# Performance work log

Hardware: AMD Instinct MI355X
Metric: run time of the kernel (lower is better)

## Reference

```python
import jax, jax.numpy as jnp
import numpy as np

N_NODES = 100000


def high_pass_filter(z, src, dst, n):
    # add self loops (PyG add_self_loops appends [i, i] edges)
    loop = jnp.arange(n, dtype=src.dtype)
    src2 = jnp.concatenate([src, loop])
    dst2 = jnp.concatenate([dst, loop])
    ones = jnp.ones(src2.shape[0], dtype=z.dtype)
    # deg = degree(edge_index[0]) -> out-degree counts per source node
    deg = jax.ops.segment_sum(ones, src2, num_segments=n)
    # mean aggregation at target nodes: out[i] = mean_{(j->i)} z[j]
    msg_sum = jax.ops.segment_sum(z[src2], dst2, num_segments=n)
    cnt = jax.ops.segment_sum(ones, dst2, num_segments=n)
    mean_out = msg_sum / cnt[:, None]  # cnt >= 1 thanks to self loops
    return z - mean_out / deg[:, None]


def setup_inputs() -> dict:
    key = jax.random.key(0)
    k = jax.random.split(key, 8)
    d = 64
    E = 1200000
    x = jax.random.normal(k[0], (N_NODES, d), dtype=jnp.float32)
    edge_index = jax.random.randint(k[1], (2, E), 0, N_NODES, dtype=jnp.int64)
    s = 1.0 / np.sqrt(d)
    W1 = jax.random.uniform(k[2], (d, d), jnp.float32, -s, s)
    b1 = jax.random.uniform(k[3], (d,), jnp.float32, -s, s)
    W2 = jax.random.uniform(k[4], (d, d), jnp.float32, -s, s)
    b2 = jax.random.uniform(k[5], (d,), jnp.float32, -s, s)
    W3 = jax.random.uniform(k[6], (d, d), jnp.float32, -s, s)
    b3 = jax.random.uniform(k[7], (d,), jnp.float32, -s, s)
    return {"x": x, "edge_index": edge_index, "W1": W1, "b1": b1,
            "W2": W2, "b2": b2, "W3": W3, "b3": b3}


def reference(x, edge_index, W1, b1, W2, b2, W3, b3):
    src, dst = edge_index[0], edge_index[1]
    n = x.shape[0]
    z = jax.nn.relu(x @ W1 + b1)
    z = high_pass_filter(z, src, dst, n)
    z = jax.nn.relu(z @ W2 + b2)
    z = high_pass_filter(z, src, dst, n)
    z = jax.nn.relu(z @ W3 + b3)
    return z
```

## Files before the change

kernel.cpp:

```cpp
#include <hip/hip_runtime.h>

#define D 64
#define CAP 48
#define CAPB 3584
#define BIN_CHUNK 2048

typedef unsigned int uint;
typedef unsigned short ushort;

__device__ __forceinline__ ushort f2bf(float f) {
    uint u = __float_as_uint(f);
    return (ushort)((u + 0x7FFFu + ((u >> 16) & 1u)) >> 16);
}

__global__ __launch_bounds__(256) void k_bin2(
    const int* __restrict__ src, const int* __restrict__ dst, int E, int nb,
    int* __restrict__ gcur, int* __restrict__ binD, int* __restrict__ binS)
{
    __shared__ int curD[512], curS[512];
    const int t = threadIdx.x;
    for (int i = t; i < nb; i += 256) { curD[i] = 0; curS[i] = 0; }
    __syncthreads();

    const int e0 = blockIdx.x * BIN_CHUNK;
    int sv[8], dv[8];
#pragma unroll
    for (int i = 0; i < 8; ++i) {
        int e = e0 + i * 256 + t;
        if (e < E) {
            sv[i] = src[e]; dv[i] = dst[e];
            atomicAdd(&curD[dv[i] >> 8], 1);
            atomicAdd(&curS[sv[i] >> 8], 1);
        } else {
            sv[i] = -1;
        }
    }
    __syncthreads();
    for (int i = t; i < nb; i += 256) {
        int c = curD[i]; curD[i] = c ? atomicAdd(&gcur[i], c) : 0;
        c = curS[i];     curS[i] = c ? atomicAdd(&gcur[nb + i], c) : 0;
    }
    __syncthreads();
#pragma unroll
    for (int i = 0; i < 8; ++i) {
        if (sv[i] >= 0) {
            int b = dv[i] >> 8;
            int pos = atomicAdd(&curD[b], 1);
            if (pos < CAPB) binD[(size_t)b * CAPB + pos] = ((dv[i] & 255) << 17) | sv[i];
            b = sv[i] >> 8;
            pos = atomicAdd(&curS[b], 1);
            if (pos < CAPB) binS[(size_t)b * CAPB + pos] = sv[i] & 255;
        }
    }
}

__global__ __launch_bounds__(256) void k_finish(
    const int* __restrict__ gcur, const int* __restrict__ binD,
    const int* __restrict__ binS, int n, int nb,
    int* __restrict__ csr, int* __restrict__ icnt, float* __restrict__ inv)
{
    __shared__ int cur[256], od[256];
    const int b = blockIdx.x, t = threadIdx.x;
    cur[t] = 0; od[t] = 0;
    __syncthreads();

    int cntD = gcur[b]; if (cntD > CAPB) cntD = CAPB;
    const int* bb = binD + (size_t)b * CAPB;
    for (int i = t; i < cntD; i += 256) {
        int v = bb[i];
        int dloc = v >> 17;
        int pos = atomicAdd(&cur[dloc], 1);
        if (pos < CAP) csr[(size_t)((b << 8) + dloc) * CAP + pos] = v & 0x1FFFF;
    }
    int cntS = gcur[nb + b]; if (cntS > CAPB) cntS = CAPB;
    const int* bs = binS + (size_t)b * CAPB;
    for (int i = t; i < cntS; i += 256) {
        atomicAdd(&od[bs[i]], 1);
    }
    __syncthreads();
    int node = (b << 8) + t;
    if (node < n) {
        int ic = cur[t]; if (ic > CAP) ic = CAP;
        icnt[node] = ic;
        inv[node] = 1.0f / ((float)(od[t] + 1) * (float)(ic + 1));
    }
}

__global__ __launch_bounds__(256) void k_aggr(
    const float* __restrict__ zA, const ushort* __restrict__ zh,
    const int* __restrict__ icnt, const int* __restrict__ csr,
    const float* __restrict__ inv, int n, float* __restrict__ zB)
{
    int w = (blockIdx.x * 256 + threadIdx.x) >> 6;
    int lane = threadIdx.x & 63;
    int c8 = (lane & 7) << 3;
    int j = lane >> 3;
    if (w >= n) return;

    int cnt = icnt[w]; if (cnt > CAP) cnt = CAP;
    int my = (lane < cnt) ? csr[w * CAP + lane] : 0;
    int nit = (cnt + 7) >> 3;

    float a[8] = {0.f, 0.f, 0.f, 0.f, 0.f, 0.f, 0.f, 0.f};
    for (int it = 0; it < nit; ++it) {
        int e = (it << 3) + j;
        int s = __shfl(my, e, 64);
        uint4 u = *(const uint4*)(zh + (size_t)s * D + c8);
        if (e < cnt) {
            a[0] += __uint_as_float(u.x << 16);
            a[1] += __uint_as_float(u.x & 0xFFFF0000u);
            a[2] += __uint_as_float(u.y << 16);
            a[3] += __uint_as_float(u.y & 0xFFFF0000u);
            a[4] += __uint_as_float(u.z << 16);
            a[5] += __uint_as_float(u.z & 0xFFFF0000u);
            a[6] += __uint_as_float(u.w << 16);
            a[7] += __uint_as_float(u.w & 0xFFFF0000u);
        }
    }
#pragma unroll
    for (int m = 8; m <= 32; m <<= 1) {
#pragma unroll
        for (int i = 0; i < 8; ++i) a[i] += __shfl_xor(a[i], m, 64);
    }

    if (j == 0) {
        float iv = inv[w];
        const float* zr = zA + (size_t)w * D + c8;
        float4 s0 = *(const float4*)zr;
        float4 s1 = *(const float4*)(zr + 4);
        float4 o0, o1;
        o0.x = fmaf(-(a[0] + s0.x), iv, s0.x);
        o0.y = fmaf(-(a[1] + s0.y), iv, s0.y);
        o0.z = fmaf(-(a[2] + s0.z), iv, s0.z);
        o0.w = fmaf(-(a[3] + s0.w), iv, s0.w);
        o1.x = fmaf(-(a[4] + s1.x), iv, s1.x);
        o1.y = fmaf(-(a[5] + s1.y), iv, s1.y);
        o1.z = fmaf(-(a[6] + s1.z), iv, s1.z);
        o1.w = fmaf(-(a[7] + s1.w), iv, s1.w);
        float* zo = zB + (size_t)w * D + c8;
        *(float4*)zo = o0;
        *(float4*)(zo + 4) = o1;
    }
}

#define LDS_STRIDE 68

__global__ __launch_bounds__(256) void k_gemm(
    const float* z, const float* __restrict__ W, const float* __restrict__ bias,
    float* out, ushort* zh_out, int n)
{
    __shared__ float sX[64 * LDS_STRIDE];
    __shared__ float sWT[64 * LDS_STRIDE];

    const int t = threadIdx.x;
    const int row0 = blockIdx.x * 64;

    for (int i = 0; i < 4; ++i) {
        int s = i * 256 + t;
        int k = s >> 4;
        int c4 = (s & 15) << 2;
        float4 w = ((const float4*)W)[s];
        sWT[(c4 + 0) * LDS_STRIDE + k] = w.x;
        sWT[(c4 + 1) * LDS_STRIDE + k] = w.y;
        sWT[(c4 + 2) * LDS_STRIDE + k] = w.z;
        sWT[(c4 + 3) * LDS_STRIDE + k] = w.w;
    }
    for (int i = 0; i < 4; ++i) {
        int s = i * 256 + t;
        int r = s >> 4;
        int grow = row0 + r;
        float4 v = make_float4(0.f, 0.f, 0.f, 0.f);
        if (grow < n) v = ((const float4*)(z + (size_t)grow * D))[s & 15];
        *((float4*)(sX + r * LDS_STRIDE + ((s & 15) << 2))) = v;
    }
    __syncthreads();

    const int tc = (t & 15) << 2;
    const int tr = (t >> 4) << 2;

    float acc[4][4] = {};
#define DOT4(a_, w_, acc_) \
    acc_ = fmaf((a_).x, (w_).x, fmaf((a_).y, (w_).y, fmaf((a_).z, (w_).z, fmaf((a_).w, (w_).w, acc_))))

    for (int k4 = 0; k4 < 16; ++k4) {
        float4 a0 = *(const float4*)(sX + (tr + 0) * LDS_STRIDE + (k4 << 2));
        float4 a1 = *(const float4*)(sX + (tr + 1) * LDS_STRIDE + (k4 << 2));
        float4 a2 = *(const float4*)(sX + (tr + 2) * LDS_STRIDE + (k4 << 2));
        float4 a3 = *(const float4*)(sX + (tr + 3) * LDS_STRIDE + (k4 << 2));
        float4 w0 = *(const float4*)(sWT + (tc + 0) * LDS_STRIDE + (k4 << 2));
        float4 w1 = *(const float4*)(sWT + (tc + 1) * LDS_STRIDE + (k4 << 2));
        float4 w2 = *(const float4*)(sWT + (tc + 2) * LDS_STRIDE + (k4 << 2));
        float4 w3 = *(const float4*)(sWT + (tc + 3) * LDS_STRIDE + (k4 << 2));
        DOT4(a0, w0, acc[0][0]); DOT4(a0, w1, acc[0][1]); DOT4(a0, w2, acc[0][2]); DOT4(a0, w3, acc[0][3]);
        DOT4(a1, w0, acc[1][0]); DOT4(a1, w1, acc[1][1]); DOT4(a1, w2, acc[1][2]); DOT4(a1, w3, acc[1][3]);
        DOT4(a2, w0, acc[2][0]); DOT4(a2, w1, acc[2][1]); DOT4(a2, w2, acc[2][2]); DOT4(a2, w3, acc[2][3]);
        DOT4(a3, w0, acc[3][0]); DOT4(a3, w1, acc[3][1]); DOT4(a3, w2, acc[3][2]); DOT4(a3, w3, acc[3][3]);
    }

    float b0 = bias[tc + 0], b1 = bias[tc + 1], b2 = bias[tc + 2], b3 = bias[tc + 3];
    for (int rr = 0; rr < 4; ++rr) {
        int grow = row0 + tr + rr;
        if (grow >= n) continue;
        float4 o;
        o.x = fmaxf(acc[rr][0] + b0, 0.f);
        o.y = fmaxf(acc[rr][1] + b1, 0.f);
        o.z = fmaxf(acc[rr][2] + b2, 0.f);
        o.w = fmaxf(acc[rr][3] + b3, 0.f);
        ((float4*)(out + (size_t)grow * D))[tc >> 2] = o;
        if (zh_out) {
            short4 h;
            h.x = (short)f2bf(o.x); h.y = (short)f2bf(o.y);
            h.z = (short)f2bf(o.z); h.w = (short)f2bf(o.w);
            *(short4*)(zh_out + (size_t)grow * D + tc) = h;
        }
    }
}

extern "C" void kernel_launch(void* const* d_in, const int* in_sizes, int n_in,
                              void* d_out, int out_size, void* d_ws, size_t ws_size,
                              hipStream_t stream) {
    const float* x  = (const float*)d_in[0];
    const int*   ei = (const int*)d_in[1];
    const float* W1 = (const float*)d_in[2];
    const float* b1 = (const float*)d_in[3];
    const float* W2 = (const float*)d_in[4];
    const float* b2 = (const float*)d_in[5];
    const float* W3 = (const float*)d_in[6];
    const float* b3 = (const float*)d_in[7];

    const int n = in_sizes[0] / D;
    const int E = in_sizes[1] / 2;
    const int* src = ei;
    const int* dst = ei + E;

    const int nb = (n + 255) >> 8;

    float*  zA   = (float*)d_ws;
    ushort* zh   = (ushort*)(zA + (size_t)n * D);
    float*  inv  = (float*)(zh + (size_t)n * D);
    int*    icnt = (int*)(inv + n);
    int*    csr  = icnt + n;
    int*    gcur = csr + (size_t)n * CAP;
    int*    binD = gcur + 2 * nb;
    int*    binS = binD + (size_t)nb * CAPB;

    float* out = (float*)d_out;
    dim3 blk(256);

    hipMemsetAsync(gcur, 0, 2 * (size_t)nb * sizeof(int), stream);

    const int bin_blocks = (E + BIN_CHUNK - 1) / BIN_CHUNK;
    k_bin2<<<dim3(bin_blocks), blk, 0, stream>>>(src, dst, E, nb, gcur, binD, binS);
    k_finish<<<dim3(nb), blk, 0, stream>>>(gcur, binD, binS, n, nb, csr, icnt, inv);

    dim3 gemm_grid((n + 63) / 64);
    dim3 aggr_grid((n + 3) / 4);

    k_gemm<<<gemm_grid, blk, 0, stream>>>(x, W1, b1, zA, zh, n);
    k_aggr<<<aggr_grid, blk, 0, stream>>>(zA, zh, icnt, csr, inv, n, zA);
    k_gemm<<<gemm_grid, blk, 0, stream>>>(zA, W2, b2, zA, zh, n);
    k_aggr<<<aggr_grid, blk, 0, stream>>>(zA, zh, icnt, csr, inv, n, zA);
    k_gemm<<<gemm_grid, blk, 0, stream>>>(zA, W3, b3, out, nullptr, n);
}
```

Before: 294.3 us.

## Merge edge binning and first GEMM into one launch, replace memset with kernel

Edge binning and the first dense layer are independent, so they now run as two halves of one grid, with block index choosing the role. This lets them overlap and removes one launch. The hipMemsetAsync is replaced by a tiny zeroing kernel, and the aggregation kernel issues its self-row and inverse-degree loads before the neighbor loop to hide latency. The cost is a larger shared-memory allocation for the binning blocks, which may lower their occupancy.

```diff
diff --git a/kernel.cpp b/kernel.cpp
--- a/kernel.cpp
+++ b/kernel.cpp
@@ -4,6 +4,7 @@
 #define CAP 48
 #define CAPB 3584
 #define BIN_CHUNK 2048
+#define LDS_STRIDE 68
 
 typedef unsigned int uint;
 typedef unsigned short ushort;
@@ -13,16 +14,21 @@
     return (ushort)((u + 0x7FFFu + ((u >> 16) & 1u)) >> 16);
 }
 
-__global__ __launch_bounds__(256) void k_bin2(
-    const int* __restrict__ src, const int* __restrict__ dst, int E, int nb,
-    int* __restrict__ gcur, int* __restrict__ binD, int* __restrict__ binS)
-{
-    __shared__ int curD[512], curS[512];
+__global__ void k_zero(int* __restrict__ p, int n) {
+    int i = blockIdx.x * blockDim.x + threadIdx.x;
+    if (i < n) p[i] = 0;
+}
+
+__device__ void bin2_body(const int* __restrict__ src, const int* __restrict__ dst,
+                          int E, int nb, int* __restrict__ gcur,
+                          int* __restrict__ binD, int* __restrict__ binS,
+                          int* curD, int* curS, int chunk)
+{
     const int t = threadIdx.x;
     for (int i = t; i < nb; i += 256) { curD[i] = 0; curS[i] = 0; }
     __syncthreads();
 
-    const int e0 = blockIdx.x * BIN_CHUNK;
+    const int e0 = chunk * BIN_CHUNK;
     int sv[8], dv[8];
 #pragma unroll
     for (int i = 0; i < 8; ++i) {
@@ -54,106 +60,12 @@
     }
 }
 
-__global__ __launch_bounds__(256) void k_finish(
-    const int* __restrict__ gcur, const int* __restrict__ binD,
-    const int* __restrict__ binS, int n, int nb,
-    int* __restrict__ csr, int* __restrict__ icnt, float* __restrict__ inv)
-{
-    __shared__ int cur[256], od[256];
-    const int b = blockIdx.x, t = threadIdx.x;
-    cur[t] = 0; od[t] = 0;
-    __syncthreads();
-
-    int cntD = gcur[b]; if (cntD > CAPB) cntD = CAPB;
-    const int* bb = binD + (size_t)b * CAPB;
-    for (int i = t; i < cntD; i += 256) {
-        int v = bb[i];
-        int dloc = v >> 17;
-        int pos = atomicAdd(&cur[dloc], 1);
-        if (pos < CAP) csr[(size_t)((b << 8) + dloc) * CAP + pos] = v & 0x1FFFF;
-    }
-    int cntS = gcur[nb + b]; if (cntS > CAPB) cntS = CAPB;
-    const int* bs = binS + (size_t)b * CAPB;
-    for (int i = t; i < cntS; i += 256) {
-        atomicAdd(&od[bs[i]], 1);
-    }
-    __syncthreads();
-    int node = (b << 8) + t;
-    if (node < n) {
-        int ic = cur[t]; if (ic > CAP) ic = CAP;
-        icnt[node] = ic;
-        inv[node] = 1.0f / ((float)(od[t] + 1) * (float)(ic + 1));
-    }
-}
-
-__global__ __launch_bounds__(256) void k_aggr(
-    const float* __restrict__ zA, const ushort* __restrict__ zh,
-    const int* __restrict__ icnt, const int* __restrict__ csr,
-    const float* __restrict__ inv, int n, float* __restrict__ zB)
-{
-    int w = (blockIdx.x * 256 + threadIdx.x) >> 6;
-    int lane = threadIdx.x & 63;
-    int c8 = (lane & 7) << 3;
-    int j = lane >> 3;
-    if (w >= n) return;
-
-    int cnt = icnt[w]; if (cnt > CAP) cnt = CAP;
-    int my = (lane < cnt) ? csr[w * CAP + lane] : 0;
-    int nit = (cnt + 7) >> 3;
-
-    float a[8] = {0.f, 0.f, 0.f, 0.f, 0.f, 0.f, 0.f, 0.f};
-    for (int it = 0; it < nit; ++it) {
-        int e = (it << 3) + j;
-        int s = __shfl(my, e, 64);
-        uint4 u = *(const uint4*)(zh + (size_t)s * D + c8);
-        if (e < cnt) {
-            a[0] += __uint_as_float(u.x << 16);
-            a[1] += __uint_as_float(u.x & 0xFFFF0000u);
-            a[2] += __uint_as_float(u.y << 16);
-            a[3] += __uint_as_float(u.y & 0xFFFF0000u);
-            a[4] += __uint_as_float(u.z << 16);
-            a[5] += __uint_as_float(u.z & 0xFFFF0000u);
-            a[6] += __uint_as_float(u.w << 16);
-            a[7] += __uint_as_float(u.w & 0xFFFF0000u);
-        }
-    }
-#pragma unroll
-    for (int m = 8; m <= 32; m <<= 1) {
-#pragma unroll
-        for (int i = 0; i < 8; ++i) a[i] += __shfl_xor(a[i], m, 64);
-    }
-
-    if (j == 0) {
-        float iv = inv[w];
-        const float* zr = zA + (size_t)w * D + c8;
-        float4 s0 = *(const float4*)zr;
-        float4 s1 = *(const float4*)(zr + 4);
-        float4 o0, o1;
-        o0.x = fmaf(-(a[0] + s0.x), iv, s0.x);
-        o0.y = fmaf(-(a[1] + s0.y), iv, s0.y);
-        o0.z = fmaf(-(a[2] + s0.z), iv, s0.z);
-        o0.w = fmaf(-(a[3] + s0.w), iv, s0.w);
-        o1.x = fmaf(-(a[4] + s1.x), iv, s1.x);
-        o1.y = fmaf(-(a[5] + s1.y), iv, s1.y);
-        o1.z = fmaf(-(a[6] + s1.z), iv, s1.z);
-        o1.w = fmaf(-(a[7] + s1.w), iv, s1.w);
-        float* zo = zB + (size_t)w * D + c8;
-        *(float4*)zo = o0;
-        *(float4*)(zo + 4) = o1;
-    }
-}
-
-#define LDS_STRIDE 68
-
-__global__ __launch_bounds__(256) void k_gemm(
-    const float* z, const float* __restrict__ W, const float* __restrict__ bias,
-    float* out, ushort* zh_out, int n)
-{
-    __shared__ float sX[64 * LDS_STRIDE];
-    __shared__ float sWT[64 * LDS_STRIDE];
-
+__device__ void gemm_body(const float* z, const float* __restrict__ W,
+                          const float* __restrict__ bias, float* out,
+                          ushort* zh_out, int n, float* sX, float* sWT, int tile)
+{
     const int t = threadIdx.x;
-    const int row0 = blockIdx.x * 64;
+    const int row0 = tile << 6;
 
     for (int i = 0; i < 4; ++i) {
         int s = i * 256 + t;
@@ -181,7 +93,6 @@
     float acc[4][4] = {};
 #define DOT4(a_, w_, acc_) \
     acc_ = fmaf((a_).x, (w_).x, fmaf((a_).y, (w_).y, fmaf((a_).z, (w_).z, fmaf((a_).w, (w_).w, acc_))))
-
     for (int k4 = 0; k4 < 16; ++k4) {
         float4 a0 = *(const float4*)(sX + (tr + 0) * LDS_STRIDE + (k4 << 2));
         float4 a1 = *(const float4*)(sX + (tr + 1) * LDS_STRIDE + (k4 << 2));
@@ -196,6 +107,7 @@
         DOT4(a2, w0, acc[2][0]); DOT4(a2, w1, acc[2][1]); DOT4(a2, w2, acc[2][2]); DOT4(a2, w3, acc[2][3]);
         DOT4(a3, w0, acc[3][0]); DOT4(a3, w1, acc[3][1]); DOT4(a3, w2, acc[3][2]); DOT4(a3, w3, acc[3][3]);
     }
+#undef DOT4
 
     float b0 = bias[tc + 0], b1 = bias[tc + 1], b2 = bias[tc + 2], b3 = bias[tc + 3];
     for (int rr = 0; rr < 4; ++rr) {
@@ -216,6 +128,127 @@
     }
 }
 
+__global__ __launch_bounds__(256) void k_binG(
+    const int* __restrict__ src, const int* __restrict__ dst, int E, int nb,
+    int* __restrict__ gcur, int* __restrict__ binD, int* __restrict__ binS,
+    int bin_blocks,
+    const float* __restrict__ x, const float* __restrict__ W1,
+    const float* __restrict__ b1, float* __restrict__ zA,
+    ushort* __restrict__ zh, int n)
+{
+    __shared__ float smem[2 * 64 * LDS_STRIDE];
+    if (blockIdx.x < bin_blocks) {
+        int* shm = (int*)smem;
+        bin2_body(src, dst, E, nb, gcur, binD, binS, shm, shm + 512, blockIdx.x);
+    } else {
+        gemm_body(x, W1, b1, zA, zh, n, smem, smem + 64 * LDS_STRIDE,
+                  blockIdx.x - bin_blocks);
+    }
+}
+
+__global__ __launch_bounds__(256) void k_gemm(
+    const float* z, const float* __restrict__ W, const float* __restrict__ bias,
+    float* out, ushort* zh_out, int n)
+{
+    __shared__ float smem[2 * 64 * LDS_STRIDE];
+    gemm_body(z, W, bias, out, zh_out, n, smem, smem + 64 * LDS_STRIDE, blockIdx.x);
+}
+
+__global__ __launch_bounds__(256) void k_finish(
+    const int* __restrict__ gcur, const int* __restrict__ binD,
+    const int* __restrict__ binS, int n, int nb,
+    int* __restrict__ csr, int* __restrict__ icnt, float* __restrict__ inv)
+{
+    __shared__ int cur[256], od[256];
+    const int b = blockIdx.x, t = threadIdx.x;
+    cur[t] = 0; od[t] = 0;
+    __syncthreads();
+
+    int cntD = gcur[b]; if (cntD > CAPB) cntD = CAPB;
+    const int* bb = binD + (size_t)b * CAPB;
+    for (int i = t; i < cntD; i += 256) {
+        int v = bb[i];
+        int dloc = v >> 17;
+        int pos = atomicAdd(&cur[dloc], 1);
+        if (pos < CAP) csr[(size_t)((b << 8) + dloc) * CAP + pos] = v & 0x1FFFF;
+    }
+    int cntS = gcur[nb + b]; if (cntS > CAPB) cntS = CAPB;
+    const int* bs = binS + (size_t)b * CAPB;
+    for (int i = t; i < cntS; i += 256) {
+        atomicAdd(&od[bs[i]], 1);
+    }
+    __syncthreads();
+    int node = (b << 8) + t;
+    if (node < n) {
+        int ic = cur[t]; if (ic > CAP) ic = CAP;
+        icnt[node] = ic;
+        inv[node] = 1.0f / ((float)(od[t] + 1) * (float)(ic + 1));
+    }
+}
+
+__global__ __launch_bounds__(256) void k_aggr(
+    const float* __restrict__ zA, const ushort* __restrict__ zh,
+    const int* __restrict__ icnt, const int* __restrict__ csr,
+    const float* __restrict__ inv, int n, float* __restrict__ zB)
+{
+    int w = (blockIdx.x * 256 + threadIdx.x) >> 6;
+    int lane = threadIdx.x & 63;
+    int c8 = (lane & 7) << 3;
+    int j = lane >> 3;
+    if (w >= n) return;
+
+    int cnt = icnt[w]; if (cnt > CAP) cnt = CAP;
+    int my = (lane < cnt) ? csr[w * CAP + lane] : 0;
+    int nit = (cnt + 7) >> 3;
+
+    float iv = 0.f;
+    float4 s0 = make_float4(0.f, 0.f, 0.f, 0.f);
+    float4 s1 = make_float4(0.f, 0.f, 0.f, 0.f);
+    if (j == 0) {
+        iv = inv[w];
+        const float* zr = zA + (size_t)w * D + c8;
+        s0 = *(const float4*)zr;
+        s1 = *(const float4*)(zr + 4);
+    }
+
+    float a[8] = {0.f, 0.f, 0.f, 0.f, 0.f, 0.f, 0.f, 0.f};
+    for (int it = 0; it < nit; ++it) {
+        int e = (it << 3) + j;
+        int s = __shfl(my, e, 64);
+        uint4 u = *(const uint4*)(zh + (size_t)s * D + c8);
+        if (e < cnt) {
+            a[0] += __uint_as_float(u.x << 16);
+            a[1] += __uint_as_float(u.x & 0xFFFF0000u);
+            a[2] += __uint_as_float(u.y << 16);
+            a[3] += __uint_as_float(u.y & 0xFFFF0000u);
+            a[4] += __uint_as_float(u.z << 16);
+            a[5] += __uint_as_float(u.z & 0xFFFF0000u);
+            a[6] += __uint_as_float(u.w << 16);
+            a[7] += __uint_as_float(u.w & 0xFFFF0000u);
+        }
+    }
+#pragma unroll
+    for (int m = 8; m <= 32; m <<= 1) {
+#pragma unroll
+        for (int i = 0; i < 8; ++i) a[i] += __shfl_xor(a[i], m, 64);
+    }
+
+    if (j == 0) {
+        float4 o0, o1;
+        o0.x = fmaf(-(a[0] + s0.x), iv, s0.x);
+        o0.y = fmaf(-(a[1] + s0.y), iv, s0.y);
+        o0.z = fmaf(-(a[2] + s0.z), iv, s0.z);
+        o0.w = fmaf(-(a[3] + s0.w), iv, s0.w);
+        o1.x = fmaf(-(a[4] + s1.x), iv, s1.x);
+        o1.y = fmaf(-(a[5] + s1.y), iv, s1.y);
+        o1.z = fmaf(-(a[6] + s1.z), iv, s1.z);
+        o1.w = fmaf(-(a[7] + s1.w), iv, s1.w);
+        float* zo = zB + (size_t)w * D + c8;
+        *(float4*)zo = o0;
+        *(float4*)(zo + 4) = o1;
+    }
+}
+
 extern "C" void kernel_launch(void* const* d_in, const int* in_sizes, int n_in,
                               void* d_out, int out_size, void* d_ws, size_t ws_size,
                               hipStream_t stream) {
@@ -247,16 +280,17 @@
     float* out = (float*)d_out;
     dim3 blk(256);
 
-    hipMemsetAsync(gcur, 0, 2 * (size_t)nb * sizeof(int), stream);
-
     const int bin_blocks = (E + BIN_CHUNK - 1) / BIN_CHUNK;
-    k_bin2<<<dim3(bin_blocks), blk, 0, stream>>>(src, dst, E, nb, gcur, binD, binS);
+    const int ntiles = (n + 63) >> 6;
+
+    k_zero<<<dim3((2 * nb + 255) / 256), blk, 0, stream>>>(gcur, 2 * nb);
+    k_binG<<<dim3(bin_blocks + ntiles), blk, 0, stream>>>(
+        src, dst, E, nb, gcur, binD, binS, bin_blocks, x, W1, b1, zA, zh, n);
     k_finish<<<dim3(nb), blk, 0, stream>>>(gcur, binD, binS, n, nb, csr, icnt, inv);
 
-    dim3 gemm_grid((n + 63) / 64);
+    dim3 gemm_grid(ntiles);
     dim3 aggr_grid((n + 3) / 4);
 
-    k_gemm<<<gemm_grid, blk, 0, stream>>>(x, W1, b1, zA, zh, n);
     k_aggr<<<aggr_grid, blk, 0, stream>>>(zA, zh, icnt, csr, inv, n, zA);
     k_gemm<<<gemm_grid, blk, 0, stream>>>(zA, W2, b2, zA, zh, n);
     k_aggr<<<aggr_grid, blk, 0, stream>>>(zA, zh, icnt, csr, inv, n, zA);
```

Result: faster. 279.9 us (-4.9%).

## Fuse neighbor aggregation into following GEMM and merge first GEMM with CSR finish

Applied to the files above, without the earlier changes.

Replaces the separate aggregate and GEMM kernels with one kernel per layer. Each wave gathers bf16 neighbor rows for 16 nodes, prefetching the next node's adjacency, and writes the filtered rows straight into the LDS tile that the GEMM then consumes. The first GEMM runs as extra blocks inside the CSR-finish kernel, and the memset becomes a small zeroing kernel. bf16 buffers are now double-buffered so a layer can write its output while neighbors still read the input. The aim is to cut launches and the fp32 intermediate write/read round trip, at the cost of far fewer waves in flight for the latency-bound gathers.

```diff
diff --git a/kernel.cpp b/kernel.cpp
--- a/kernel.cpp
+++ b/kernel.cpp
@@ -4,6 +4,7 @@
 #define CAP 48
 #define CAPB 3584
 #define BIN_CHUNK 2048
+#define LDS_STRIDE 68
 
 typedef unsigned int uint;
 typedef unsigned short ushort;
@@ -11,6 +12,11 @@
 __device__ __forceinline__ ushort f2bf(float f) {
     uint u = __float_as_uint(f);
     return (ushort)((u + 0x7FFFu + ((u >> 16) & 1u)) >> 16);
+}
+
+__global__ void k_zero(int* __restrict__ p, int n) {
+    int i = blockIdx.x * blockDim.x + threadIdx.x;
+    if (i < n) p[i] = 0;
 }
 
 __global__ __launch_bounds__(256) void k_bin2(
@@ -54,106 +60,12 @@
     }
 }
 
-__global__ __launch_bounds__(256) void k_finish(
-    const int* __restrict__ gcur, const int* __restrict__ binD,
-    const int* __restrict__ binS, int n, int nb,
-    int* __restrict__ csr, int* __restrict__ icnt, float* __restrict__ inv)
+__device__ void gemm_body(const float* z, const float* __restrict__ W,
+                          const float* __restrict__ bias, float* out,
+                          ushort* zh_out, int n, float* sX, float* sWT, int tile)
 {
-    __shared__ int cur[256], od[256];
-    const int b = blockIdx.x, t = threadIdx.x;
-    cur[t] = 0; od[t] = 0;
-    __syncthreads();
-
-    int cntD = gcur[b]; if (cntD > CAPB) cntD = CAPB;
-    const int* bb = binD + (size_t)b * CAPB;
-    for (int i = t; i < cntD; i += 256) {
-        int v = bb[i];
-        int dloc = v >> 17;
-        int pos = atomicAdd(&cur[dloc], 1);
-        if (pos < CAP) csr[(size_t)((b << 8) + dloc) * CAP + pos] = v & 0x1FFFF;
-    }
-    int cntS = gcur[nb + b]; if (cntS > CAPB) cntS = CAPB;
-    const int* bs = binS + (size_t)b * CAPB;
-    for (int i = t; i < cntS; i += 256) {
-        atomicAdd(&od[bs[i]], 1);
-    }
-    __syncthreads();
-    int node = (b << 8) + t;
-    if (node < n) {
-        int ic = cur[t]; if (ic > CAP) ic = CAP;
-        icnt[node] = ic;
-        inv[node] = 1.0f / ((float)(od[t] + 1) * (float)(ic + 1));
-    }
-}
-
-__global__ __launch_bounds__(256) void k_aggr(
-    const float* __restrict__ zA, const ushort* __restrict__ zh,
-    const int* __restrict__ icnt, const int* __restrict__ csr,
-    const float* __restrict__ inv, int n, float* __restrict__ zB)
-{
-    int w = (blockIdx.x * 256 + threadIdx.x) >> 6;
-    int lane = threadIdx.x & 63;
-    int c8 = (lane & 7) << 3;
-    int j = lane >> 3;
-    if (w >= n) return;
-
-    int cnt = icnt[w]; if (cnt > CAP) cnt = CAP;
-    int my = (lane < cnt) ? csr[w * CAP + lane] : 0;
-    int nit = (cnt + 7) >> 3;
-
-    float a[8] = {0.f, 0.f, 0.f, 0.f, 0.f, 0.f, 0.f, 0.f};
-    for (int it = 0; it < nit; ++it) {
-        int e = (it << 3) + j;
-        int s = __shfl(my, e, 64);
-        uint4 u = *(const uint4*)(zh + (size_t)s * D + c8);
-        if (e < cnt) {
-            a[0] += __uint_as_float(u.x << 16);
-            a[1] += __uint_as_float(u.x & 0xFFFF0000u);
-            a[2] += __uint_as_float(u.y << 16);
-            a[3] += __uint_as_float(u.y & 0xFFFF0000u);
-            a[4] += __uint_as_float(u.z << 16);
-            a[5] += __uint_as_float(u.z & 0xFFFF0000u);
-            a[6] += __uint_as_float(u.w << 16);
-            a[7] += __uint_as_float(u.w & 0xFFFF0000u);
-        }
-    }
-#pragma unroll
-    for (int m = 8; m <= 32; m <<= 1) {
-#pragma unroll
-        for (int i = 0; i < 8; ++i) a[i] += __shfl_xor(a[i], m, 64);
-    }
-
-    if (j == 0) {
-        float iv = inv[w];
-        const float* zr = zA + (size_t)w * D + c8;
-        float4 s0 = *(const float4*)zr;
-        float4 s1 = *(const float4*)(zr + 4);
-        float4 o0, o1;
-        o0.x = fmaf(-(a[0] + s0.x), iv, s0.x);
-        o0.y = fmaf(-(a[1] + s0.y), iv, s0.y);
-        o0.z = fmaf(-(a[2] + s0.z), iv, s0.z);
-        o0.w = fmaf(-(a[3] + s0.w), iv, s0.w);
-        o1.x = fmaf(-(a[4] + s1.x), iv, s1.x);
-        o1.y = fmaf(-(a[5] + s1.y), iv, s1.y);
-        o1.z = fmaf(-(a[6] + s1.z), iv, s1.z);
-        o1.w = fmaf(-(a[7] + s1.w), iv, s1.w);
-        float* zo = zB + (size_t)w * D + c8;
-        *(float4*)zo = o0;
-        *(float4*)(zo + 4) = o1;
-    }
-}
-
-#define LDS_STRIDE 68
-
-__global__ __launch_bounds__(256) void k_gemm(
-    const float* z, const float* __restrict__ W, const float* __restrict__ bias,
-    float* out, ushort* zh_out, int n)
-{
-    __shared__ float sX[64 * LDS_STRIDE];
-    __shared__ float sWT[64 * LDS_STRIDE];
-
     const int t = threadIdx.x;
-    const int row0 = blockIdx.x * 64;
+    const int row0 = tile << 6;
 
     for (int i = 0; i < 4; ++i) {
         int s = i * 256 + t;
@@ -181,7 +93,6 @@
     float acc[4][4] = {};
 #define DOT4(a_, w_, acc_) \
     acc_ = fmaf((a_).x, (w_).x, fmaf((a_).y, (w_).y, fmaf((a_).z, (w_).z, fmaf((a_).w, (w_).w, acc_))))
-
     for (int k4 = 0; k4 < 16; ++k4) {
         float4 a0 = *(const float4*)(sX + (tr + 0) * LDS_STRIDE + (k4 << 2));
         float4 a1 = *(const float4*)(sX + (tr + 1) * LDS_STRIDE + (k4 << 2));
@@ -196,6 +107,7 @@
         DOT4(a2, w0, acc[2][0]); DOT4(a2, w1, acc[2][1]); DOT4(a2, w2, acc[2][2]); DOT4(a2, w3, acc[2][3]);
         DOT4(a3, w0, acc[3][0]); DOT4(a3, w1, acc[3][1]); DOT4(a3, w2, acc[3][2]); DOT4(a3, w3, acc[3][3]);
     }
+#undef DOT4
 
     float b0 = bias[tc + 0], b1 = bias[tc + 1], b2 = bias[tc + 2], b3 = bias[tc + 3];
     for (int rr = 0; rr < 4; ++rr) {
@@ -216,6 +128,185 @@
     }
 }
 
+__global__ __launch_bounds__(256) void k_finishG(
+    const int* __restrict__ gcur, const int* __restrict__ binD,
+    const int* __restrict__ binS, int n, int nb,
+    int* __restrict__ csr, int* __restrict__ icnt, float* __restrict__ inv,
+    const float* __restrict__ x, const float* __restrict__ W1,
+    const float* __restrict__ b1, float* __restrict__ zA,
+    ushort* __restrict__ zh, int ntiles)
+{
+    __shared__ float smem[2 * 64 * LDS_STRIDE];
+    if (blockIdx.x >= nb) {
+        gemm_body(x, W1, b1, zA, zh, n, smem, smem + 64 * LDS_STRIDE,
+                  blockIdx.x - nb);
+        return;
+    }
+    int* cur = (int*)smem;
+    int* od  = (int*)smem + 256;
+    const int b = blockIdx.x, t = threadIdx.x;
+    cur[t] = 0; od[t] = 0;
+    __syncthreads();
+
+    int cntD = gcur[b]; if (cntD > CAPB) cntD = CAPB;
+    const int* bb = binD + (size_t)b * CAPB;
+    for (int i = t; i < cntD; i += 256) {
+        int v = bb[i];
+        int dloc = v >> 17;
+        int pos = atomicAdd(&cur[dloc], 1);
+        if (pos < CAP) csr[(size_t)((b << 8) + dloc) * CAP + pos] = v & 0x1FFFF;
+    }
+    int cntS = gcur[nb + b]; if (cntS > CAPB) cntS = CAPB;
+    const int* bs = binS + (size_t)b * CAPB;
+    for (int i = t; i < cntS; i += 256) {
+        atomicAdd(&od[bs[i]], 1);
+    }
+    __syncthreads();
+    int node = (b << 8) + t;
+    if (node < n) {
+        int ic = cur[t]; if (ic > CAP) ic = CAP;
+        icnt[node] = ic;
+        inv[node] = 1.0f / ((float)(od[t] + 1) * (float)(ic + 1));
+    }
+}
+
+__global__ __launch_bounds__(256) void k_AG(
+    const float* zA, const ushort* __restrict__ zh_in,
+    const int* __restrict__ icnt, const int* __restrict__ csr,
+    const float* __restrict__ inv,
+    const float* __restrict__ W, const float* __restrict__ bias,
+    float* outz, ushort* __restrict__ zh_out, int n)
+{
+    __shared__ float sX[64 * LDS_STRIDE];
+    __shared__ float sWT[64 * LDS_STRIDE];
+    const int t = threadIdx.x;
+    const int row0 = blockIdx.x << 6;
+
+    for (int i = 0; i < 4; ++i) {
+        int s = i * 256 + t;
+        int k = s >> 4;
+        int c4 = (s & 15) << 2;
+        float4 w = ((const float4*)W)[s];
+        sWT[(c4 + 0) * LDS_STRIDE + k] = w.x;
+        sWT[(c4 + 1) * LDS_STRIDE + k] = w.y;
+        sWT[(c4 + 2) * LDS_STRIDE + k] = w.z;
+        sWT[(c4 + 3) * LDS_STRIDE + k] = w.w;
+    }
+
+    const int lane = t & 63;
+    const int wv = t >> 6;
+    const int c8 = (lane & 7) << 3;
+    const int j = lane >> 3;
+    const int wbase = row0 + wv * 16;
+
+    int cntN = 0, myN = 0;
+    if (wbase < n) {
+        cntN = icnt[wbase]; if (cntN > CAP) cntN = CAP;
+        myN = (lane < cntN) ? csr[wbase * CAP + lane] : 0;
+    }
+
+    for (int i = 0; i < 16; ++i) {
+        const int w = wbase + i;
+        const int r = wv * 16 + i;
+        const int cnt = cntN;
+        const int my = myN;
+        if (i < 15) {
+            int wn = w + 1;
+            if (wn < n) {
+                int c = icnt[wn]; if (c > CAP) c = CAP;
+                cntN = c;
+                myN = (lane < c) ? csr[wn * CAP + lane] : 0;
+            } else { cntN = 0; myN = 0; }
+        }
+        if (w < n) {
+            float a[8] = {0.f, 0.f, 0.f, 0.f, 0.f, 0.f, 0.f, 0.f};
+            const int nit = (cnt + 7) >> 3;
+            for (int it = 0; it < nit; ++it) {
+                int e = (it << 3) + j;
+                int s = __shfl(my, e, 64);
+                uint4 u = *(const uint4*)(zh_in + (size_t)s * D + c8);
+                if (e < cnt) {
+                    a[0] += __uint_as_float(u.x << 16);
+                    a[1] += __uint_as_float(u.x & 0xFFFF0000u);
+                    a[2] += __uint_as_float(u.y << 16);
+                    a[3] += __uint_as_float(u.y & 0xFFFF0000u);
+                    a[4] += __uint_as_float(u.z << 16);
+                    a[5] += __uint_as_float(u.z & 0xFFFF0000u);
+                    a[6] += __uint_as_float(u.w << 16);
+                    a[7] += __uint_as_float(u.w & 0xFFFF0000u);
+                }
+            }
+#pragma unroll
+            for (int m = 8; m <= 32; m <<= 1) {
+#pragma unroll
+                for (int i2 = 0; i2 < 8; ++i2) a[i2] += __shfl_xor(a[i2], m, 64);
+            }
+            if (j == 0) {
+                float iv = inv[w];
+                const float* zr = zA + (size_t)w * D + c8;
+                float4 s0 = *(const float4*)zr;
+                float4 s1 = *(const float4*)(zr + 4);
+                float4 o0, o1;
+                o0.x = fmaf(-(a[0] + s0.x), iv, s0.x);
+                o0.y = fmaf(-(a[1] + s0.y), iv, s0.y);
+                o0.z = fmaf(-(a[2] + s0.z), iv, s0.z);
+                o0.w = fmaf(-(a[3] + s0.w), iv, s0.w);
+                o1.x = fmaf(-(a[4] + s1.x), iv, s1.x);
+                o1.y = fmaf(-(a[5] + s1.y), iv, s1.y);
+                o1.z = fmaf(-(a[6] + s1.z), iv, s1.z);
+                o1.w = fmaf(-(a[7] + s1.w), iv, s1.w);
+                *(float4*)(sX + r * LDS_STRIDE + c8) = o0;
+                *(float4*)(sX + r * LDS_STRIDE + c8 + 4) = o1;
+            }
+        } else if (j == 0) {
+            float4 zz = make_float4(0.f, 0.f, 0.f, 0.f);
+            *(float4*)(sX + r * LDS_STRIDE + c8) = zz;
+            *(float4*)(sX + r * LDS_STRIDE + c8 + 4) = zz;
+        }
+    }
+    __syncthreads();
+
+    const int tc = (t & 15) << 2;
+    const int tr = (t >> 4) << 2;
+
+    float acc[4][4] = {};
+#define DOT4(a_, w_, acc_) \
+    acc_ = fmaf((a_).x, (w_).x, fmaf((a_).y, (w_).y, fmaf((a_).z, (w_).z, fmaf((a_).w, (w_).w, acc_))))
+    for (int k4 = 0; k4 < 16; ++k4) {
+        float4 a0 = *(const float4*)(sX + (tr + 0) * LDS_STRIDE + (k4 << 2));
+        float4 a1 = *(const float4*)(sX + (tr + 1) * LDS_STRIDE + (k4 << 2));
+        float4 a2 = *(const float4*)(sX + (tr + 2) * LDS_STRIDE + (k4 << 2));
+        float4 a3 = *(const float4*)(sX + (tr + 3) * LDS_STRIDE + (k4 << 2));
+        float4 w0 = *(const float4*)(sWT + (tc + 0) * LDS_STRIDE + (k4 << 2));
+        float4 w1 = *(const float4*)(sWT + (tc + 1) * LDS_STRIDE + (k4 << 2));
+        float4 w2 = *(const float4*)(sWT + (tc + 2) * LDS_STRIDE + (k4 << 2));
+        float4 w3 = *(const float4*)(sWT + (tc + 3) * LDS_STRIDE + (k4 << 2));
+        DOT4(a0, w0, acc[0][0]); DOT4(a0, w1, acc[0][1]); DOT4(a0, w2, acc[0][2]); DOT4(a0, w3, acc[0][3]);
+        DOT4(a1, w0, acc[1][0]); DOT4(a1, w1, acc[1][1]); DOT4(a1, w2, acc[1][2]); DOT4(a1, w3, acc[1][3]);
+        DOT4(a2, w0, acc[2][0]); DOT4(a2, w1, acc[2][1]); DOT4(a2, w2, acc[2][2]); DOT4(a2, w3, acc[2][3]);
+        DOT4(a3, w0, acc[3][0]); DOT4(a3, w1, acc[3][1]); DOT4(a3, w2, acc[3][2]); DOT4(a3, w3, acc[3][3]);
+    }
+#undef DOT4
+
+    float b0 = bias[tc + 0], b1 = bias[tc + 1], b2 = bias[tc + 2], b3 = bias[tc + 3];
+    for (int rr = 0; rr < 4; ++rr) {
+        int grow = row0 + tr + rr;
+        if (grow >= n) continue;
+        float4 o;
+        o.x = fmaxf(acc[rr][0] + b0, 0.f);
+        o.y = fmaxf(acc[rr][1] + b1, 0.f);
+        o.z = fmaxf(acc[rr][2] + b2, 0.f);
+        o.w = fmaxf(acc[rr][3] + b3, 0.f);
+        ((float4*)(outz + (size_t)grow * D))[tc >> 2] = o;
+        if (zh_out) {
+            short4 h;
+            h.x = (short)f2bf(o.x); h.y = (short)f2bf(o.y);
+            h.z = (short)f2bf(o.z); h.w = (short)f2bf(o.w);
+            *(short4*)(zh_out + (size_t)grow * D + tc) = h;
+        }
+    }
+}
+
 extern "C" void kernel_launch(void* const* d_in, const int* in_sizes, int n_in,
                               void* d_out, int out_size, void* d_ws, size_t ws_size,
                               hipStream_t stream) {
@@ -236,8 +327,9 @@
     const int nb = (n + 255) >> 8;
 
     float*  zA   = (float*)d_ws;
-    ushort* zh   = (ushort*)(zA + (size_t)n * D);
-    float*  inv  = (float*)(zh + (size_t)n * D);
+    ushort* zh_a = (ushort*)(zA + (size_t)n * D);
+    ushort* zh_b = zh_a + (size_t)n * D;
+    float*  inv  = (float*)(zh_b + (size_t)n * D);
     int*    icnt = (int*)(inv + n);
     int*    csr  = icnt + n;
     int*    gcur = csr + (size_t)n * CAP;
@@ -247,18 +339,15 @@
     float* out = (float*)d_out;
     dim3 blk(256);
 
-    hipMemsetAsync(gcur, 0, 2 * (size_t)nb * sizeof(int), stream);
-
     const int bin_blocks = (E + BIN_CHUNK - 1) / BIN_CHUNK;
+    const int ntiles = (n + 63) >> 6;
+
+    k_zero<<<dim3((2 * nb + 255) / 256), blk, 0, stream>>>(gcur, 2 * nb);
     k_bin2<<<dim3(bin_blocks), blk, 0, stream>>>(src, dst, E, nb, gcur, binD, binS);
-    k_finish<<<dim3(nb), blk, 0, stream>>>(gcur, binD, binS, n, nb, csr, icnt, inv);
-
-    dim3 gemm_grid((n + 63) / 64);
-    dim3 aggr_grid((n + 3) / 4);
-
-    k_gemm<<<gemm_grid, blk, 0, stream>>>(x, W1, b1, zA, zh, n);
-    k_aggr<<<aggr_grid, blk, 0, stream>>>(zA, zh, icnt, csr, inv, n, zA);
-    k_gemm<<<gemm_grid, blk, 0, stream>>>(zA, W2, b2, zA, zh, n);
-    k_aggr<<<aggr_grid, blk, 0, stream>>>(zA, zh, icnt, csr, inv, n, zA);
-    k_gemm<<<gemm_grid, blk, 0, stream>>>(zA, W3, b3, out, nullptr, n);
-}
+    k_finishG<<<dim3(nb + ntiles), blk, 0, stream>>>(
+        gcur, binD, binS, n, nb, csr, icnt, inv, x, W1, b1, zA, zh_a, ntiles);
+    k_AG<<<dim3(ntiles), blk, 0, stream>>>(zA, zh_a, icnt, csr, inv,
+                                           W2, b2, zA, zh_b, n);
+    k_AG<<<dim3(ntiles), blk, 0, stream>>>(zA, zh_b, icnt, csr, inv,
+                                           W3, b3, out, nullptr, n);
+}
```

Result: slower. 315.8 us (+7.3%).
